# Optimization experiments

Measured on AMD Instinct MI355X. Metric: run time of the kernel, lower is better.

The kernel has to match this reference:

```python
import jax, jax.numpy as jnp
import numpy as np

B, N, D = 4, 1024, 256
NH, P = 8, 7
K = P * P
HH, WW = 64, 64


def setup_inputs() -> dict:
    key = jax.random.key(0)
    ks = jax.random.split(key, 12)
    w = lambda i, shp: (jax.random.normal(ks[i], shp, jnp.float32) * 0.02)
    return {
        "decoder_embed": jax.random.normal(ks[0], (B, N, D), jnp.float32),
        "ref_boxes": jax.random.uniform(ks[1], (B, N, 4), jnp.float32),
        "memory": jax.random.normal(ks[2], (B, D, HH, WW), jnp.float32),
        "Wq": w(3, (D, D)), "bq": jnp.zeros((D,), jnp.float32),
        "Wk": w(4, (D, D)), "bk": jnp.zeros((D,), jnp.float32),
        "Wv": w(5, (D, D)), "bv": jnp.zeros((D,), jnp.float32),
        "Wo": w(6, (D, D)), "bo": jnp.zeros((D,), jnp.float32),
        "Woff1": w(7, (D, D)), "boff1": jnp.zeros((D,), jnp.float32),
        "Woff2": w(8, (D, 2 * K)), "boff2": jnp.zeros((2 * K,), jnp.float32),
        "sigma": jnp.float32(0.1),
    }


def reference(decoder_embed, ref_boxes, memory, Wq, bq, Wk, bk, Wv, bv,
              Wo, bo, Woff1, boff1, Woff2, boff2, sigma):
    Bb, Nn, Dm = decoder_embed.shape
    _, C, H, W = memory.shape
    nh, p = NH, P
    kk = p * p
    hd = Dm // nh

    # local grid in normalized [-1,1] coords (k,) each
    coords = jnp.linspace(-(p - 1) / 2.0, (p - 1) / 2.0, p, dtype=jnp.float32)
    gx, gy = jnp.meshgrid(coords, coords, indexing='xy')
    lx = gx.reshape(-1) * (2.0 / max(W - 1, 1))
    ly = gy.reshape(-1) * (2.0 / max(H - 1, 1))

    # queries: (B, nh, N, hd)
    q = (decoder_embed @ Wq + bq).reshape(Bb, Nn, nh, hd).transpose(0, 2, 1, 3)

    # predicted offsets: (B, N, k, 2), tanh * sigma
    h = jax.nn.relu(decoder_embed @ Woff1 + boff1)
    off = jnp.tanh(h @ Woff2 + boff2).reshape(Bb, Nn, kk, 2) * sigma

    cx = ref_boxes[..., 0] * 2.0 - 1.0
    cy = ref_boxes[..., 1] * 2.0 - 1.0
    sx = jnp.clip(cx[..., None] + lx + off[..., 0], -1.0, 1.0)  # (B,N,k)
    sy = jnp.clip(cy[..., None] + ly + off[..., 1], -1.0, 1.0)

    # bilinear sample (grid_sample, align_corners=True); coords in-bounds after clip
    x = (sx + 1.0) * 0.5 * (W - 1)
    y = (sy + 1.0) * 0.5 * (H - 1)
    x0 = jnp.floor(x); y0 = jnp.floor(y)
    fx = x - x0; fy = y - y0
    x0i = jnp.clip(x0.astype(jnp.int32), 0, W - 1)
    x1i = jnp.clip(x0i + 1, 0, W - 1)
    y0i = jnp.clip(y0.astype(jnp.int32), 0, H - 1)
    y1i = jnp.clip(y0i + 1, 0, H - 1)

    mem = memory.transpose(0, 2, 3, 1)  # (B,H,W,C)
    bidx = jnp.arange(Bb)[:, None, None]
    gather = lambda yi, xi: mem[bidx, yi, xi]  # (B,N,k,C)
    sampled = (gather(y0i, x0i) * ((1 - fx) * (1 - fy))[..., None]
               + gather(y0i, x1i) * (fx * (1 - fy))[..., None]
               + gather(y1i, x0i) * ((1 - fx) * fy)[..., None]
               + gather(y1i, x1i) * (fx * fy)[..., None])  # (B,N,k,C)

    k_all = (sampled @ Wk + bk).reshape(Bb, Nn, kk, nh, hd).transpose(0, 3, 1, 2, 4)
    v_all = (sampled @ Wv + bv).reshape(Bb, Nn, kk, nh, hd).transpose(0, 3, 1, 2, 4)

    scores = jnp.einsum('bhnd,bhnkd->bhnk', q, k_all) / jnp.sqrt(jnp.float32(hd))
    attn = jax.nn.softmax(scores, axis=-1)  # (B,nh,N,k)
    out_heads = jnp.einsum('bhnk,bhnkd->bhnd', attn, v_all)
    out = out_heads.transpose(0, 2, 1, 3).reshape(Bb, Nn, Dm) @ Wo + bo
    return out, attn
```

## Files before the change

### kernel.cpp

```cpp
#include <hip/hip_runtime.h>
#include <hip/hip_bf16.h>
#include <math.h>

#define DEV __device__ __forceinline__

typedef __attribute__((ext_vector_type(8))) short bf16x8;
typedef __attribute__((ext_vector_type(4))) float f32x4;

constexpr int BB = 4, NQ1 = 1024, DM = 256, KK = 49;
constexpr int HWP = 4096;
constexpr int NQT = 4096;

DEV float bflo(unsigned u) { return __uint_as_float(u << 16); }
DEV float bfhi(unsigned u) { return __uint_as_float(u & 0xffff0000u); }
DEV unsigned pack2(float a, float b) {
    __hip_bfloat162 h2;
    h2.x = __float2bfloat16(a);
    h2.y = __float2bfloat16(b);
    unsigned u;
    __builtin_memcpy(&u, &h2, 4);
    return u;
}
DEV ushort f2bf(float a) {
    __hip_bfloat16 h = __float2bfloat16(a);
    ushort u;
    __builtin_memcpy(&u, &h, 2);
    return u;
}

__global__ __launch_bounds__(256) void k_prep(
    const float* __restrict__ X, ushort* __restrict__ Xbf,
    const float* __restrict__ mem, ushort* __restrict__ memT,
    const float* __restrict__ Wq, const float* __restrict__ Wk,
    const float* __restrict__ bq, ushort* __restrict__ WqkT, float* __restrict__ bqk,
    const float* __restrict__ Wv, const float* __restrict__ Wo,
    const float* __restrict__ bv, const float* __restrict__ bo,
    ushort* __restrict__ WvoT, float* __restrict__ bvo,
    const float* __restrict__ Woff1, ushort* __restrict__ W1t,
    const float* __restrict__ Woff2, ushort* __restrict__ W2t) {
    __shared__ float smem[32 * 33];
    const int blk = blockIdx.x;
    const int t = threadIdx.x;

    if (blk < 512) {
        int i = (blk * 256 + t) * 8;
        float4 a = *(const float4*)&X[i];
        float4 b = *(const float4*)&X[i + 4];
        uint4 pk;
        pk.x = pack2(a.x, a.y);
        pk.y = pack2(a.z, a.w);
        pk.z = pack2(b.x, b.y);
        pk.w = pack2(b.z, b.w);
        *(uint4*)&Xbf[i] = pk;
    } else if (blk < 4608) {
        int r = blk - 512;
        int p0 = (r & 127) * 32;
        int c0 = ((r >> 7) & 7) * 32;
        int b = r >> 10;
        int tx = t & 31, ty = t >> 5;
        float (*tile)[33] = (float(*)[33])smem;
        const float* s = mem + ((size_t)b * DM + c0) * HWP + p0;
#pragma unroll
        for (int i = 0; i < 32; i += 8) tile[ty + i][tx] = s[(size_t)(ty + i) * HWP + tx];
        __syncthreads();
        ushort* d = memT + ((size_t)b * HWP + p0) * DM + c0;
#pragma unroll
        for (int i = 0; i < 32; i += 8)
            d[(size_t)(ty + i) * DM + tx] = f2bf(tile[tx][ty + i]);
    } else if (blk < 6656) {
        int hc = blk - 4608;
        int h = hc >> 8, c = hc & 255;
        if (t < 32) smem[t] = Wk[(size_t)c * 256 + h * 32 + t];
        __syncthreads();
        const float* wq = Wq + (size_t)t * 256 + h * 32;
        float acc = 0.f;
#pragma unroll
        for (int j = 0; j < 32; ++j) acc += wq[j] * smem[j];
        WqkT[(size_t)hc * 256 + t] = f2bf(acc);
        if (t == 0) {
            float bacc = 0.f;
#pragma unroll
            for (int j = 0; j < 32; ++j) bacc += bq[h * 32 + j] * smem[j];
            bqk[hc] = bacc;
        }
    } else if (blk < 6912) {
        int e = blk - 6656;
        smem[t] = Wo[(size_t)t * 256 + e];
        __syncthreads();
        for (int hc = t; hc < 2048; hc += 256) {
            int h = hc >> 8, c = hc & 255;
            const float* wv = Wv + (size_t)c * 256 + h * 32;
            const float* wo = &smem[h * 32];
            float acc = 0.f;
#pragma unroll
            for (int j = 0; j < 32; ++j) acc += wv[j] * wo[j];
            WvoT[(size_t)e * 2048 + hc] = f2bf(acc);
        }
        if (t == 0) {
            float bacc = bo[e];
#pragma unroll 8
            for (int d = 0; d < 256; ++d) bacc += bv[d] * smem[d];
            bvo[e] = bacc;
        }
    } else {
        const float* src;
        ushort* dst;
        int K = 256, N, r;
        if (blk < 6976) { r = blk - 6912; src = Woff1; dst = W1t; N = 256; }
        else            { r = blk - 6976; src = Woff2; dst = W2t; N = 98; }
        int nblk = (N + 31) / 32;
        int n0 = (r % nblk) * 32, k0 = (r / nblk) * 32;
        int tx = t & 31, ty = t >> 5;
        float (*tile)[33] = (float(*)[33])smem;
#pragma unroll
        for (int i = 0; i < 32; i += 8)
            if (n0 + tx < N) tile[ty + i][tx] = src[(size_t)(k0 + ty + i) * N + n0 + tx];
        __syncthreads();
#pragma unroll
        for (int i = 0; i < 32; i += 8)
            if (n0 + ty + i < N)
                dst[(size_t)(n0 + ty + i) * K + k0 + tx] = f2bf(tile[tx][ty + i]);
    }
}

template <int TM, int TN, int BK, int ACT, int OUTBF>
__global__ __launch_bounds__(256) void gemm_bf16(
    const ushort* __restrict__ A, const ushort* __restrict__ Bt,
    const float* __restrict__ bias, void* __restrict__ Cout,
    int N, int K, int ldc, const float* __restrict__ sclp) {
    constexpr int SL = BK / 8;
    __shared__ ushort As[TM][BK];
    __shared__ ushort Bs[TN][BK];
    const int t = threadIdx.x;
    const int lane = t & 63, wid = t >> 6;
    const int wr = wid >> 1, wc = wid & 1;
    const int m0 = blockIdx.y * TM, n0 = blockIdx.x * TN;
    constexpr int FM = TM / 32, FN = TN / 32, KS = BK / 32;
    f32x4 acc[FM][FN];
#pragma unroll
    for (int i = 0; i < FM; ++i)
#pragma unroll
        for (int j = 0; j < FN; ++j) acc[i][j] = (f32x4){0.f, 0.f, 0.f, 0.f};

    const int l15 = lane & 15, lkg = lane >> 4;

    for (int k0 = 0; k0 < K; k0 += BK) {
        constexpr int NA = TM * SL / 256;
#pragma unroll
        for (int i = 0; i < NA; ++i) {
            int idx = t + i * 256;
            int m = idx / SL, sl = idx % SL;
            int ss = sl ^ ((m >> 1) & (SL - 1));
            *(uint4*)&As[m][ss * 8] = *(const uint4*)&A[(size_t)(m0 + m) * K + k0 + sl * 8];
        }
        constexpr int NB = TN * SL / 256;
#pragma unroll
        for (int i = 0; i < NB; ++i) {
            int idx = t + i * 256;
            int nn = idx / SL, sl = idx % SL;
            int ss = sl ^ ((nn >> 1) & (SL - 1));
            uint4 v = {0u, 0u, 0u, 0u};
            if (n0 + nn < N) v = *(const uint4*)&Bt[(size_t)(n0 + nn) * K + k0 + sl * 8];
            *(uint4*)&Bs[nn][ss * 8] = v;
        }
        __syncthreads();
#pragma unroll
        for (int ks = 0; ks < KS; ++ks) {
            bf16x8 af[FM], bfv[FN];
#pragma unroll
            for (int mi = 0; mi < FM; ++mi) {
                int R = wr * (TM / 2) + mi * 16 + l15;
                int ss = (lkg + ks * 4) ^ ((R >> 1) & (SL - 1));
                af[mi] = *(const bf16x8*)&As[R][ss * 8];
            }
#pragma unroll
            for (int ni = 0; ni < FN; ++ni) {
                int R = wc * (TN / 2) + ni * 16 + l15;
                int ss = (lkg + ks * 4) ^ ((R >> 1) & (SL - 1));
                bfv[ni] = *(const bf16x8*)&Bs[R][ss * 8];
            }
#pragma unroll
            for (int mi = 0; mi < FM; ++mi)
#pragma unroll
                for (int ni = 0; ni < FN; ++ni)
                    acc[mi][ni] = __builtin_amdgcn_mfma_f32_16x16x32_bf16(
                        af[mi], bfv[ni], acc[mi][ni], 0, 0, 0);
        }
        __syncthreads();
    }

    float scl = (ACT == 2) ? *sclp : 0.f;
#pragma unroll
    for (int mi = 0; mi < FM; ++mi)
#pragma unroll
        for (int ni = 0; ni < FN; ++ni) {
            int col = n0 + wc * (TN / 2) + ni * 16 + l15;
            if (col < N) {
                float bcol = bias[col];
#pragma unroll
                for (int i = 0; i < 4; ++i) {
                    int row = m0 + wr * (TM / 2) + mi * 16 + lkg * 4 + i;
                    float v = acc[mi][ni][i] + bcol;
                    if (ACT == 1) v = fmaxf(v, 0.f);
                    else if (ACT == 2) v = tanhf(v) * scl;
                    if (OUTBF)
                        ((ushort*)Cout)[(size_t)row * ldc + col] = f2bf(v);
                    else
                        ((float*)Cout)[(size_t)row * ldc + col] = v;
                }
            }
        }
}

__global__ __launch_bounds__(256) void k2_attn(
    const ushort* __restrict__ memT, const float* __restrict__ refb,
    const float* __restrict__ OFFb, const ushort* __restrict__ QKb,
    ushort* __restrict__ AGG, float* __restrict__ attnOut) {
    __shared__ unsigned samp[49 * 132];
    __shared__ unsigned pxb[4][4][64];
    __shared__ float attnL[49][8];
    const int t = threadIdx.x;
    const int wid = t >> 6, lane = t & 63;
    const int qu = __builtin_amdgcn_readfirstlane((int)((blockIdx.x & 7) * 512 + (blockIdx.x >> 3)));
    const int b = qu >> 10, n = qu & 1023;
    const bool act = lane < KK;

    const float cx = refb[(size_t)qu * 4 + 0] * 2.f - 1.f;
    const float cy = refb[(size_t)qu * 4 + 1] * 2.f - 1.f;
    float ox = 0.f, oy = 0.f;
    if (act) {
        float2 o2 = *(const float2*)&OFFb[(size_t)qu * 98 + 2 * lane];
        ox = o2.x;
        oy = o2.y;
    }
    float sx = fminf(fmaxf(cx + (float)((lane % 7) - 3) * (2.f / 63.f) + ox, -1.f), 1.f);
    float sy = fminf(fmaxf(cy + (float)(((lane / 7) % 7) - 3) * (2.f / 63.f) + oy, -1.f), 1.f);
    float xf = (sx + 1.f) * 31.5f, yf = (sy + 1.f) * 31.5f;
    float x0f = floorf(xf), y0f = floorf(yf);
    float fx = xf - x0f, fy = yf - y0f;
    int x0 = min(max((int)x0f, 0), 63), y0 = min(max((int)y0f, 0), 63);
    int x1 = min(x0 + 1, 63), y1 = min(y0 + 1, 63);
    float w00 = (1.f - fx) * (1.f - fy), w01 = fx * (1.f - fy);
    float w10 = (1.f - fx) * fy, w11 = fx * fy;

    const ushort* mb = memT + (size_t)b * HWP * DM;
    const ushort* qk0 = QKb + (size_t)__builtin_amdgcn_readfirstlane(qu * 2048 + wid * 64);

    float p[8];
#pragma unroll
    for (int h = 0; h < 8; ++h) p[h] = 0.f;

    if (act) {
        const ushort* p00 = mb + (size_t)(y0 * 64 + x0) * DM + wid * 64;
        const ushort* p01 = mb + (size_t)(y0 * 64 + x1) * DM + wid * 64;
        const ushort* p10 = mb + (size_t)(y1 * 64 + x0) * DM + wid * 64;
        const ushort* p11 = mb + (size_t)(y1 * 64 + x1) * DM + wid * 64;
        unsigned* srow = &samp[lane * 132 + wid * 32];
#pragma unroll 4
        for (int cc = 0; cc < 64; cc += 8) {
            uint4 u00 = *(const uint4*)(p00 + cc);
            uint4 u01 = *(const uint4*)(p01 + cc);
            uint4 u10 = *(const uint4*)(p10 + cc);
            uint4 u11 = *(const uint4*)(p11 + cc);
            const unsigned* a00 = (const unsigned*)&u00;
            const unsigned* a01 = (const unsigned*)&u01;
            const unsigned* a10 = (const unsigned*)&u10;
            const unsigned* a11 = (const unsigned*)&u11;
            float s[8];
#pragma unroll
            for (int q = 0; q < 4; ++q) {
                s[2 * q] = w00 * bflo(a00[q]) + w01 * bflo(a01[q]) +
                           w10 * bflo(a10[q]) + w11 * bflo(a11[q]);
                s[2 * q + 1] = w00 * bfhi(a00[q]) + w01 * bfhi(a01[q]) +
                               w10 * bfhi(a10[q]) + w11 * bfhi(a11[q]);
            }
            uint4 pk;
            pk.x = pack2(s[0], s[1]);
            pk.y = pack2(s[2], s[3]);
            pk.z = pack2(s[4], s[5]);
            pk.w = pack2(s[6], s[7]);
            *(uint4*)&srow[cc / 2] = pk;
#pragma unroll
            for (int h = 0; h < 8; ++h) {
                uint4 qv = *(const uint4*)(qk0 + h * 256 + cc);
                const unsigned* aq = (const unsigned*)&qv;
                p[h] += s[0] * bflo(aq[0]) + s[1] * bfhi(aq[0]) +
                        s[2] * bflo(aq[1]) + s[3] * bfhi(aq[1]) +
                        s[4] * bflo(aq[2]) + s[5] * bfhi(aq[2]) +
                        s[6] * bflo(aq[3]) + s[7] * bfhi(aq[3]);
            }
        }
#pragma unroll
        for (int hp = 0; hp < 4; ++hp)
            pxb[wid][hp][lane] = pack2(p[2 * hp], p[2 * hp + 1]);
    }
    __syncthreads();

    float p0 = 0.f, p1 = 0.f;
    if (act) {
#pragma unroll
        for (int w = 0; w < 4; ++w) {
            unsigned u = pxb[w][wid][lane];
            p0 += bflo(u);
            p1 += bfhi(u);
        }
    }
    const float scl = 0.17677669529663687f;
    float s0 = act ? p0 * scl : -INFINITY;
    float s1 = act ? p1 * scl : -INFINITY;
    float m0v = s0, m1v = s1;
#pragma unroll
    for (int off = 32; off; off >>= 1) {
        m0v = fmaxf(m0v, __shfl_xor(m0v, off));
        m1v = fmaxf(m1v, __shfl_xor(m1v, off));
    }
    float e0 = act ? __expf(s0 - m0v) : 0.f;
    float e1 = act ? __expf(s1 - m1v) : 0.f;
    float sum0 = e0, sum1 = e1;
#pragma unroll
    for (int off = 32; off; off >>= 1) {
        sum0 += __shfl_xor(sum0, off);
        sum1 += __shfl_xor(sum1, off);
    }
    float at0 = e0 / sum0, at1 = e1 / sum1;
    if (act) {
        attnL[lane][2 * wid] = at0;
        attnL[lane][2 * wid + 1] = at1;
        attnOut[((size_t)(b * 8 + 2 * wid) * 1024 + n) * 49 + lane] = at0;
        attnOut[((size_t)(b * 8 + 2 * wid + 1) * 1024 + n) * 49 + lane] = at1;
    }
    __syncthreads();

    const int c = t;
    float acc[8];
#pragma unroll
    for (int h = 0; h < 8; ++h) acc[h] = 0.f;
#pragma unroll 7
    for (int k = 0; k < KK; ++k) {
        unsigned d = samp[k * 132 + (c >> 1)];
        float sv = (c & 1) ? bfhi(d) : bflo(d);
        float4 a0 = *(const float4*)&attnL[k][0];
        float4 a1 = *(const float4*)&attnL[k][4];
        acc[0] += a0.x * sv;
        acc[1] += a0.y * sv;
        acc[2] += a0.z * sv;
        acc[3] += a0.w * sv;
        acc[4] += a1.x * sv;
        acc[5] += a1.y * sv;
        acc[6] += a1.z * sv;
        acc[7] += a1.w * sv;
    }
    ushort* ag = AGG + (size_t)qu * 2048 + c;
#pragma unroll
    for (int h = 0; h < 8; ++h) ag[h * 256] = f2bf(acc[h]);
}

extern "C" void kernel_launch(void* const* d_in, const int* in_sizes, int n_in,
                              void* d_out, int out_size, void* d_ws, size_t ws_size,
                              hipStream_t stream) {
    (void)in_sizes; (void)n_in; (void)out_size; (void)ws_size;
    const float* X     = (const float*)d_in[0];
    const float* refb  = (const float*)d_in[1];
    const float* mem   = (const float*)d_in[2];
    const float* Wq    = (const float*)d_in[3];
    const float* bq    = (const float*)d_in[4];
    const float* Wk    = (const float*)d_in[5];
    const float* Wv    = (const float*)d_in[7];
    const float* bv    = (const float*)d_in[8];
    const float* Wo    = (const float*)d_in[9];
    const float* bo    = (const float*)d_in[10];
    const float* Woff1 = (const float*)d_in[11];
    const float* boff1 = (const float*)d_in[12];
    const float* Woff2 = (const float*)d_in[13];
    const float* boff2 = (const float*)d_in[14];
    const float* sigma = (const float*)d_in[15];

    float* out  = (float*)d_out;
    float* attn = out + (size_t)NQT * DM;

    float* ws = (float*)d_ws;
    ushort* memT  = (ushort*)(ws + 0);
    ushort* Xbf   = (ushort*)(ws + 2097152);
    ushort* WqkT  = (ushort*)(ws + 2621440);
    float*  bqk   = ws + 2883584;
    ushort* WvoT  = (ushort*)(ws + 2885632);
    float*  bvo   = ws + 3147776;
    ushort* W1t   = (ushort*)(ws + 3148032);
    ushort* W2t   = (ushort*)(ws + 3180800);
    ushort* QKbf  = (ushort*)(ws + 3193344);
    ushort* Hbf   = (ushort*)(ws + 7387648);
    float*  OFFb  = ws + 7911936;
    ushort* AGGb  = (ushort*)(ws + 8313344);

    k_prep<<<7008, 256, 0, stream>>>(X, Xbf, mem, memT, Wq, Wk, bq, WqkT, bqk,
                                     Wv, Wo, bv, bo, WvoT, bvo, Woff1, W1t, Woff2, W2t);

    gemm_bf16<128, 64, 64, 0, 1><<<dim3(32, 32), 256, 0, stream>>>(
        Xbf, WqkT, bqk, QKbf, 2048, 256, 2048, nullptr);
    gemm_bf16<64, 64, 64, 1, 1><<<dim3(4, 64), 256, 0, stream>>>(
        Xbf, W1t, boff1, Hbf, 256, 256, 256, nullptr);
    gemm_bf16<64, 64, 64, 2, 0><<<dim3(2, 64), 256, 0, stream>>>(
        Hbf, W2t, boff2, OFFb, 98, 256, 98, sigma);

    k2_attn<<<4096, 256, 0, stream>>>(memT, refb, OFFb, QKbf, AGGb, attn);

    gemm_bf16<64, 32, 64, 0, 0><<<dim3(8, 64), 256, 0, stream>>>(
        AGGb, WvoT, bvo, out, 256, 2048, 256, nullptr);
}
```

Before: 250.2 us.

## Compute attention scores with MFMA from LDS-staged samples instead of scalar dot products

```diff
diff --git a/kernel.cpp b/kernel.cpp
--- a/kernel.cpp
+++ b/kernel.cpp
@@ -216,11 +216,12 @@
     const ushort* __restrict__ memT, const float* __restrict__ refb,
     const float* __restrict__ OFFb, const ushort* __restrict__ QKb,
     ushort* __restrict__ AGG, float* __restrict__ attnOut) {
-    __shared__ unsigned samp[49 * 132];
-    __shared__ unsigned pxb[4][4][64];
+    __shared__ ushort samp[64][264];
+    __shared__ float sL[64][9];
     __shared__ float attnL[49][8];
     const int t = threadIdx.x;
     const int wid = t >> 6, lane = t & 63;
+    const int l15 = lane & 15, lkg = lane >> 4;
     const int qu = __builtin_amdgcn_readfirstlane((int)((blockIdx.x & 7) * 512 + (blockIdx.x >> 3)));
     const int b = qu >> 10, n = qu & 1023;
     const bool act = lane < KK;
@@ -244,19 +245,14 @@
     float w10 = (1.f - fx) * fy, w11 = fx * fy;
 
     const ushort* mb = memT + (size_t)b * HWP * DM;
-    const ushort* qk0 = QKb + (size_t)__builtin_amdgcn_readfirstlane(qu * 2048 + wid * 64);
-
-    float p[8];
-#pragma unroll
-    for (int h = 0; h < 8; ++h) p[h] = 0.f;
 
     if (act) {
         const ushort* p00 = mb + (size_t)(y0 * 64 + x0) * DM + wid * 64;
         const ushort* p01 = mb + (size_t)(y0 * 64 + x1) * DM + wid * 64;
         const ushort* p10 = mb + (size_t)(y1 * 64 + x0) * DM + wid * 64;
         const ushort* p11 = mb + (size_t)(y1 * 64 + x1) * DM + wid * 64;
-        unsigned* srow = &samp[lane * 132 + wid * 32];
-#pragma unroll 4
+        unsigned* srow = (unsigned*)&samp[lane][0] + wid * 32;
+#pragma unroll 2
         for (int cc = 0; cc < 64; cc += 8) {
             uint4 u00 = *(const uint4*)(p00 + cc);
             uint4 u01 = *(const uint4*)(p01 + cc);
@@ -280,30 +276,33 @@
             pk.z = pack2(s[4], s[5]);
             pk.w = pack2(s[6], s[7]);
             *(uint4*)&srow[cc / 2] = pk;
-#pragma unroll
-            for (int h = 0; h < 8; ++h) {
-                uint4 qv = *(const uint4*)(qk0 + h * 256 + cc);
-                const unsigned* aq = (const unsigned*)&qv;
-                p[h] += s[0] * bflo(aq[0]) + s[1] * bfhi(aq[0]) +
-                        s[2] * bflo(aq[1]) + s[3] * bfhi(aq[1]) +
-                        s[4] * bflo(aq[2]) + s[5] * bfhi(aq[2]) +
-                        s[6] * bflo(aq[3]) + s[7] * bfhi(aq[3]);
-            }
-        }
-#pragma unroll
-        for (int hp = 0; hp < 4; ++hp)
-            pxb[wid][hp][lane] = pack2(p[2 * hp], p[2 * hp + 1]);
+        }
+    }
+    __syncthreads();
+
+    {
+        f32x4 sacc = (f32x4){0.f, 0.f, 0.f, 0.f};
+        const ushort* qkq = QKb + (size_t)qu * 2048;
+#pragma unroll
+        for (int ks = 0; ks < 8; ++ks) {
+            bf16x8 a = *(const bf16x8*)&samp[wid * 16 + l15][ks * 32 + lkg * 8];
+            uint4 bz = {0u, 0u, 0u, 0u};
+            if (l15 < 8) bz = *(const uint4*)&qkq[l15 * 256 + ks * 32 + lkg * 8];
+            bf16x8 bvv;
+            __builtin_memcpy(&bvv, &bz, 16);
+            sacc = __builtin_amdgcn_mfma_f32_16x16x32_bf16(a, bvv, sacc, 0, 0, 0);
+        }
+        if (l15 < 8) {
+#pragma unroll
+            for (int i = 0; i < 4; ++i) sL[wid * 16 + lkg * 4 + i][l15] = sacc[i];
+        }
     }
     __syncthreads();
 
     float p0 = 0.f, p1 = 0.f;
     if (act) {
-#pragma unroll
-        for (int w = 0; w < 4; ++w) {
-            unsigned u = pxb[w][wid][lane];
-            p0 += bflo(u);
-            p1 += bfhi(u);
-        }
+        p0 = sL[lane][2 * wid];
+        p1 = sL[lane][2 * wid + 1];
     }
     const float scl = 0.17677669529663687f;
     float s0 = act ? p0 * scl : -INFINITY;
@@ -337,7 +336,7 @@
     for (int h = 0; h < 8; ++h) acc[h] = 0.f;
 #pragma unroll 7
     for (int k = 0; k < KK; ++k) {
-        unsigned d = samp[k * 132 + (c >> 1)];
+        unsigned d = ((const unsigned*)&samp[k][0])[c >> 1];
         float sv = (c & 1) ? bfhi(d) : bflo(d);
         float4 a0 = *(const float4*)&attnL[k][0];
         float4 a1 = *(const float4*)&attnL[k][4];
```

After: 250.2 us. Within noise of the previous version (-0.0%).
